# Kernel tuning notes

Hardware: AMD Instinct MI355X
Metric: run time of the kernel (lower is better)

The kernel has to match this reference:

```python
import jax, jax.numpy as jnp
import numpy as np

# static config (matches init_kwargs and spatial_shapes input)
SPATIAL = ((100, 100), (50, 50), (25, 25), (13, 13))  # (H, W) per level
D_MODEL, N_HEADS, N_LEVELS, N_POINTS, D_FFN = 256, 8, 4, 4, 1024
D_HEAD = D_MODEL // N_HEADS
LEN_IN = sum(h * w for h, w in SPATIAL)
LEVEL_START = np.cumsum([0] + [h * w for h, w in SPATIAL])[:-1]


def setup_inputs() -> dict:
    key = jax.random.key(0)
    ks = jax.random.split(key, 12)
    N = 2
    f = lambda k, shape, s=0.02: jax.random.normal(k, shape, jnp.float32) * s
    return {
        "src": jax.random.normal(ks[0], (N, LEN_IN, D_MODEL), jnp.float32),
        "pos": jax.random.normal(ks[1], (N, LEN_IN, D_MODEL), jnp.float32),
        "reference_points": jax.random.uniform(ks[2], (N, LEN_IN, N_LEVELS, 2), jnp.float32),
        "spatial_shapes": jnp.asarray(SPATIAL, jnp.int32),
        "level_start_index": jnp.asarray(LEVEL_START, jnp.int32),
        "W_value": f(ks[3], (D_MODEL, D_MODEL)),
        "b_value": jnp.zeros((D_MODEL,), jnp.float32),
        "W_off": f(ks[4], (D_MODEL, N_HEADS * N_LEVELS * N_POINTS * 2)),
        "b_off": f(ks[5], (N_HEADS * N_LEVELS * N_POINTS * 2,), 0.5),
        "W_attn": f(ks[6], (D_MODEL, N_HEADS * N_LEVELS * N_POINTS)),
        "b_attn": jnp.zeros((N_HEADS * N_LEVELS * N_POINTS,), jnp.float32),
        "W_out": f(ks[7], (D_MODEL, D_MODEL)),
        "b_out": jnp.zeros((D_MODEL,), jnp.float32),
        "W1": f(ks[8], (D_MODEL, D_FFN)),
        "b1": jnp.zeros((D_FFN,), jnp.float32),
        "W2": f(ks[9], (D_FFN, D_MODEL)),
        "b2": jnp.zeros((D_MODEL,), jnp.float32),
        "g1": jnp.ones((D_MODEL,), jnp.float32),
        "be1": jnp.zeros((D_MODEL,), jnp.float32),
        "g2": jnp.ones((D_MODEL,), jnp.float32),
        "be2": jnp.zeros((D_MODEL,), jnp.float32),
    }


def _ln(x, g, b, eps=1e-5):
    mu = x.mean(-1, keepdims=True)
    var = ((x - mu) ** 2).mean(-1, keepdims=True)
    return (x - mu) * jax.lax.rsqrt(var + eps) * g + b


def _bilinear(v, loc, H, W):
    # v: [N, heads, H*W, Dh]; loc: [N, Lq, heads, P, 2] normalized to [0,1]
    # replicates F.grid_sample(align_corners=False, padding_mode='zeros') with grid=2*loc-1
    N, Lq, Hh, P, _ = loc.shape
    x = loc[..., 0] * W - 0.5
    y = loc[..., 1] * H - 0.5
    x0 = jnp.floor(x)
    y0 = jnp.floor(y)
    wx1 = x - x0
    wy1 = y - y0
    x0i = x0.astype(jnp.int32)
    y0i = y0.astype(jnp.int32)
    out = jnp.zeros((N, Lq, Hh, P, v.shape[-1]), v.dtype)
    for dy, dx in ((0, 0), (0, 1), (1, 0), (1, 1)):
        xi = x0i + dx
        yi = y0i + dy
        w = (wx1 if dx else 1.0 - wx1) * (wy1 if dy else 1.0 - wy1)
        valid = (xi >= 0) & (xi < W) & (yi >= 0) & (yi < H)
        idx = jnp.clip(yi, 0, H - 1) * W + jnp.clip(xi, 0, W - 1)  # [N,Lq,Hh,P]
        idx = idx.transpose(0, 2, 1, 3).reshape(N, Hh, Lq * P)
        g = jax.vmap(jax.vmap(lambda vm, im: vm[im]))(v, idx)  # [N,Hh,Lq*P,Dh]
        g = g.reshape(N, Hh, Lq, P, -1).transpose(0, 2, 1, 3, 4)
        out = out + (w * valid)[..., None] * g
    return out


def reference(src, pos, reference_points, spatial_shapes, level_start_index,
              W_value, b_value, W_off, b_off, W_attn, b_attn, W_out, b_out,
              W1, b1, W2, b2, g1, be1, g2, be2):
    N, Lq, _ = src.shape
    value = (src @ W_value + b_value).reshape(N, Lq, N_HEADS, D_HEAD)
    q = src + pos  # with_pos_embed
    off = (q @ W_off + b_off).reshape(N, Lq, N_HEADS, N_LEVELS, N_POINTS, 2)
    attn = (q @ W_attn + b_attn).reshape(N, Lq, N_HEADS, N_LEVELS * N_POINTS)
    attn = jax.nn.softmax(attn, axis=-1).reshape(N, Lq, N_HEADS, N_LEVELS, N_POINTS)
    # offset_normalizer = (W, H) per level
    normalizer = jnp.asarray([[w, h] for h, w in SPATIAL], jnp.float32)
    loc = reference_points[:, :, None, :, None, :] + off / normalizer[None, None, None, :, None, :]
    out = jnp.zeros((N, Lq, N_HEADS, D_HEAD), jnp.float32)
    for l, (H, W) in enumerate(SPATIAL):
        s = int(LEVEL_START[l])
        v_l = value[:, s:s + H * W].transpose(0, 2, 1, 3)  # [N, heads, H*W, Dh]
        samp = _bilinear(v_l, loc[:, :, :, l], H, W)       # [N, Lq, heads, P, Dh]
        out = out + jnp.einsum('nqhp,nqhpc->nqhc', attn[:, :, :, l], samp)
    src2 = out.reshape(N, Lq, D_MODEL) @ W_out + b_out
    x = _ln(src + src2, g1, be1)
    ffn = jax.nn.relu(x @ W1 + b1) @ W2 + b2
    return _ln(x + ffn, g2, be2)
```

## Files before the change

### kernel.cpp

```cpp
#include <hip/hip_runtime.h>
#include <hip/hip_bf16.h>
#include <cstdint>

#define D_MODEL   256
#define N_HEADS   8
#define N_LEVELS  4
#define N_POINTS  4
#define D_FFN     1024
#define D_HEAD    32
#define LEN_IN    13294
#define NBATCH    2
#define M_TOK     (NBATCH * LEN_IN)
#define M_PAD     26624

__constant__ int c_lvl_h[4] = {100, 50, 25, 13};
__constant__ int c_lvl_w[4] = {100, 50, 25, 13};
__constant__ int c_lvl_s[4] = {0, 10000, 12500, 13125};

typedef __attribute__((ext_vector_type(8))) __bf16 bf16x8;
typedef __attribute__((ext_vector_type(4))) __bf16 bf16x4;
typedef __attribute__((ext_vector_type(4))) float  f32x4;
typedef __attribute__((ext_vector_type(4))) uint32_t u32x4;

__device__ __forceinline__ float bflo(uint32_t w) { return __uint_as_float(w << 16); }
__device__ __forceinline__ float bfhi(uint32_t w) { return __uint_as_float(w & 0xffff0000u); }

__device__ __forceinline__ void lds_direct16(const void* g, void* l) {
    __builtin_amdgcn_global_load_lds(
        (const __attribute__((address_space(1))) uint32_t*)(uintptr_t)g,
        (__attribute__((address_space(3))) uint32_t*)(uintptr_t)l,
        16, 0, 0);
}

__global__ __launch_bounds__(256) void prep(
    const float* __restrict__ s0, const float* __restrict__ s1, const float* __restrict__ s2,
    const float* __restrict__ s3, const float* __restrict__ s4, const float* __restrict__ s5,
    __bf16* __restrict__ d0, __bf16* __restrict__ d1, __bf16* __restrict__ d2,
    __bf16* __restrict__ d3, __bf16* __restrict__ d4, __bf16* __restrict__ d5,
    const float* __restrict__ b_off, const float* __restrict__ b_attn,
    float* __restrict__ bias_oa,
    const float4* __restrict__ src, const float4* __restrict__ pos,
    bf16x4* __restrict__ sb, bf16x4* __restrict__ qb, int n4)
{
    const int tid = threadIdx.x;
    const int b = blockIdx.x;
    if (b >= 737) {
        const int i = (b - 737) * 256 + tid;
        if (i >= n4) return;
        const float4 s = src[i];
        const float4 p = pos[i];
        bf16x4 sv = { (__bf16)s.x, (__bf16)s.y, (__bf16)s.z, (__bf16)s.w };
        bf16x4 qv = { (__bf16)(s.x + p.x), (__bf16)(s.y + p.y),
                      (__bf16)(s.z + p.z), (__bf16)(s.w + p.w) };
        sb[i] = sv;
        qb[i] = qv;
        return;
    }
    if (b == 736) {
        if (tid < 256) bias_oa[tid] = b_off[tid];
        if (tid < 128) bias_oa[256 + tid] = b_attn[tid];
        return;
    }
    const int tx = tid & 31;
    const int ty = tid >> 5;
    const int starts[7] = {0, 64, 128, 160, 224, 480, 736};
    const int Ks[6] = {256, 256, 256, 256, 256, 1024};
    const int Ns[6] = {256, 256, 128, 256, 1024, 256};
    const float* srcs[6] = {s0, s1, s2, s3, s4, s5};
    __bf16* dsts[6] = {d0, d1, d2, d3, d4, d5};
    int i = 0;
    while (b >= starts[i + 1]) ++i;
    const int t = b - starts[i];
    const int K = Ks[i], N = Ns[i];
    const float* W = srcs[i];
    __bf16* Wt = dsts[i];
    const int ntx = N >> 5;
    const int n0 = (t % ntx) * 32;
    const int k0 = (t / ntx) * 32;

    __shared__ float tl[32][33];
    #pragma unroll
    for (int j = 0; j < 4; ++j)
        tl[ty + j * 8][tx] = W[(size_t)(k0 + ty + j * 8) * N + n0 + tx];
    __syncthreads();
    #pragma unroll
    for (int j = 0; j < 4; ++j)
        Wt[(size_t)(n0 + ty + j * 8) * K + k0 + tx] = (__bf16)tl[tx][ty + j * 8];
}

template <bool RELU, int K, bool HEADMAJOR>
__device__ __forceinline__ void gemm_core(
    const __bf16* __restrict__ A, const __bf16* __restrict__ Bt,
    const float* __restrict__ bias, __bf16* __restrict__ C,
    int M, int N, int bm, int bn)
{
    __shared__ __bf16 smem[17408];
    __bf16* As = smem;
    __bf16* Bs = smem + 8192;

    const int tid  = threadIdx.x;
    const int lane = tid & 63;
    const int wv   = tid >> 6;
    const int wm   = (wv >> 1) * 64;
    const int wn   = (wv & 1) * 64;
    const int srow = lane >> 2;
    const int skc  = (lane & 3) * 8;
    const int fm   = lane & 15;
    const int fko  = (lane >> 4) * 8;

    f32x4 acc[4][4] = {};

    for (int k0 = 0; k0 < K; k0 += 64) {
        #pragma unroll
        for (int p = 0; p < 2; ++p) {
            #pragma unroll
            for (int c = 0; c < 2; ++c) {
                const int r = wv * 32 + c * 16;
                lds_direct16(A  + (size_t)(bm + r + srow) * K + k0 + p * 32 + skc, As + p * 4096 + r * 32);
                lds_direct16(Bt + (size_t)(bn + r + srow) * K + k0 + p * 32 + skc, Bs + p * 4096 + r * 32);
            }
        }
        __syncthreads();

        #pragma unroll
        for (int p = 0; p < 2; ++p) {
            bf16x8 af[4], bfr[4];
            #pragma unroll
            for (int t = 0; t < 4; ++t) {
                af[t]  = *(const bf16x8*)(As + p * 4096 + (wm + t * 16 + fm) * 32 + fko);
                bfr[t] = *(const bf16x8*)(Bs + p * 4096 + (wn + t * 16 + fm) * 32 + fko);
            }
            #pragma unroll
            for (int mt = 0; mt < 4; ++mt)
                #pragma unroll
                for (int nt = 0; nt < 4; ++nt)
                    acc[mt][nt] = __builtin_amdgcn_mfma_f32_16x16x32_bf16(
                        af[mt], bfr[nt], acc[mt][nt], 0, 0, 0);
        }
        __syncthreads();
    }

    const int ecol = lane & 15;
    const int erow = (lane >> 4) * 4;
    #pragma unroll
    for (int nt = 0; nt < 4; ++nt) {
        const int cl = wn + nt * 16 + ecol;
        const float bv = bias[bn + cl];
        #pragma unroll
        for (int mt = 0; mt < 4; ++mt) {
            #pragma unroll
            for (int r = 0; r < 4; ++r) {
                const int rl = wm + mt * 16 + erow + r;
                float v = acc[mt][nt][r] + bv;
                if (RELU) v = fmaxf(v, 0.f);
                smem[rl * 136 + cl] = (__bf16)v;
            }
        }
    }
    __syncthreads();
    #pragma unroll
    for (int rr = 0; rr < 8; ++rr) {
        const int idx = rr * 256 + tid;
        if (HEADMAJOR) {
            const int plane = idx >> 9;
            const int row   = (idx >> 2) & 127;
            const int ch4   = idx & 3;
            if (bm + row < M)
                *(bf16x8*)(C + ((size_t)((bn >> 5) + plane) * M_PAD + (bm + row)) * 32 + ch4 * 8) =
                    *(const bf16x8*)(smem + row * 136 + plane * 32 + ch4 * 8);
        } else {
            const int row = idx >> 4;
            const int ch  = idx & 15;
            if (bm + row < M)
                *(bf16x8*)(C + (size_t)(bm + row) * N + bn + ch * 8) =
                    *(const bf16x8*)(smem + row * 136 + ch * 8);
        }
    }
}

__global__ __launch_bounds__(256) void gemm_front(
    const __bf16* __restrict__ A0, const __bf16* __restrict__ B0,
    const float* __restrict__ bi0, __bf16* __restrict__ C0,
    const __bf16* __restrict__ A1, const __bf16* __restrict__ B1,
    const float* __restrict__ bi1, __bf16* __restrict__ C1, int M)
{
    const int bx = blockIdx.x;
    if (bx < 2)
        gemm_core<false, 256, true>(A0, B0, bi0, C0, M, 256, blockIdx.y * 128, bx * 128);
    else
        gemm_core<false, 256, false>(A1, B1, bi1, C1, M, 384, blockIdx.y * 128, (bx - 2) * 128);
}

__global__ __launch_bounds__(256) void gemm_ffn1(
    const __bf16* __restrict__ A, const __bf16* __restrict__ Bt,
    const float* __restrict__ bias, __bf16* __restrict__ C, int M)
{
    gemm_core<true, 256, false>(A, Bt, bias, C, M, 1024, blockIdx.y * 128, blockIdx.x * 128);
}

template <typename OutT, int K>
__global__ __launch_bounds__(256, 4) void gemm_ln(
    const __bf16* __restrict__ A, const __bf16* __restrict__ Bt,
    const float* __restrict__ bias, const __bf16* __restrict__ res,
    const float* __restrict__ gamma, const float* __restrict__ beta,
    OutT* __restrict__ Cout, int M)
{
    __shared__ __bf16 smem[2][9216];
    __shared__ float lnsum[32][4];
    __shared__ float lnsq[32][4];
    __shared__ float lnstat[32][2];

    const int tid  = threadIdx.x;
    const int lane = tid & 63;
    const int wv   = tid >> 6;
    const int bm   = blockIdx.x * 32;
    const int wn   = wv * 64;
    const int srow = lane >> 2;
    const int skc  = (lane & 3) * 8;
    const int fm   = lane & 15;
    const int fko  = (lane >> 4) * 8;

    f32x4 acc[2][4] = {};

    auto stage = [&](int b, int k0) {
        __bf16* As = smem[b];
        __bf16* Bs = smem[b] + 1024;
        if (tid < 128)
            lds_direct16(A + (size_t)(bm + (tid >> 2)) * K + k0 + (tid & 3) * 8,
                         As + tid * 8);
        #pragma unroll
        for (int c = 0; c < 4; ++c) {
            const int r = wv * 64 + c * 16;
            lds_direct16(Bt + (size_t)(r + srow) * K + k0 + skc, Bs + r * 32);
        }
    };
    auto compute = [&](int b) {
        const __bf16* As = smem[b];
        const __bf16* Bs = smem[b] + 1024;
        bf16x8 af[2], bfr[4];
        #pragma unroll
        for (int mt = 0; mt < 2; ++mt)
            af[mt] = *(const bf16x8*)(As + (mt * 16 + fm) * 32 + fko);
        #pragma unroll
        for (int nt = 0; nt < 4; ++nt)
            bfr[nt] = *(const bf16x8*)(Bs + (wn + nt * 16 + fm) * 32 + fko);
        #pragma unroll
        for (int mt = 0; mt < 2; ++mt)
            #pragma unroll
            for (int nt = 0; nt < 4; ++nt)
                acc[mt][nt] = __builtin_amdgcn_mfma_f32_16x16x32_bf16(
                    af[mt], bfr[nt], acc[mt][nt], 0, 0, 0);
    };

    stage(0, 0);
    __syncthreads();
    int cur = 0;
    for (int k0 = 32; k0 < K; k0 += 32) {
        stage(cur ^ 1, k0);
        compute(cur);
        __syncthreads();
        cur ^= 1;
    }
    compute(cur);

    const int ecol = lane & 15;
    const int erow = (lane >> 4) * 4;

    float g4[4], b4[4];
    #pragma unroll
    for (int nt = 0; nt < 4; ++nt) {
        const int col = wn + nt * 16 + ecol;
        g4[nt] = gamma[col];
        b4[nt] = beta[col];
        const float bv = bias[col];
        #pragma unroll
        for (int mt = 0; mt < 2; ++mt) {
            #pragma unroll
            for (int r = 0; r < 4; ++r) {
                const int row = bm + mt * 16 + erow + r;
                acc[mt][nt][r] += bv + (float)res[(size_t)row * 256 + col];
            }
        }
    }

    #pragma unroll
    for (int mt = 0; mt < 2; ++mt) {
        #pragma unroll
        for (int r = 0; r < 4; ++r) {
            float s  = acc[mt][0][r] + acc[mt][1][r] + acc[mt][2][r] + acc[mt][3][r];
            float s2 = acc[mt][0][r] * acc[mt][0][r] + acc[mt][1][r] * acc[mt][1][r]
                     + acc[mt][2][r] * acc[mt][2][r] + acc[mt][3][r] * acc[mt][3][r];
            #pragma unroll
            for (int o = 1; o < 16; o <<= 1) {
                s  += __shfl_xor(s, o);
                s2 += __shfl_xor(s2, o);
            }
            if (ecol == 0) {
                const int rl = mt * 16 + erow + r;
                lnsum[rl][wv] = s;
                lnsq[rl][wv]  = s2;
            }
        }
    }
    __syncthreads();
    if (tid < 32) {
        const float s  = lnsum[tid][0] + lnsum[tid][1] + lnsum[tid][2] + lnsum[tid][3];
        const float s2 = lnsq[tid][0] + lnsq[tid][1] + lnsq[tid][2] + lnsq[tid][3];
        const float mu = s * (1.f / 256.f);
        const float var = s2 * (1.f / 256.f) - mu * mu;
        lnstat[tid][0] = mu;
        lnstat[tid][1] = rsqrtf(var + 1e-5f);
    }
    __syncthreads();

    if constexpr (sizeof(OutT) == 2) {
        __bf16* ct = smem[0];
        #pragma unroll
        for (int mt = 0; mt < 2; ++mt) {
            #pragma unroll
            for (int r = 0; r < 4; ++r) {
                const int rl = mt * 16 + erow + r;
                const float mu = lnstat[rl][0];
                const float rs = lnstat[rl][1];
                #pragma unroll
                for (int nt = 0; nt < 4; ++nt) {
                    const int col = wn + nt * 16 + ecol;
                    ct[rl * 264 + col] = (__bf16)((acc[mt][nt][r] - mu) * rs * g4[nt] + b4[nt]);
                }
            }
        }
        __syncthreads();
        #pragma unroll
        for (int rr = 0; rr < 4; ++rr) {
            const int idx = rr * 256 + tid;
            const int row = idx >> 5;
            const int ch  = idx & 31;
            if (bm + row < M)
                *(bf16x8*)((__bf16*)Cout + (size_t)(bm + row) * 256 + ch * 8) =
                    *(const bf16x8*)(ct + row * 264 + ch * 8);
        }
    } else {
        float* ct = (float*)smem[0];
        #pragma unroll
        for (int hf = 0; hf < 2; ++hf) {
            const int mt = hf;
            #pragma unroll
            for (int r = 0; r < 4; ++r) {
                const int rl   = mt * 16 + erow + r;
                const int rloc = erow + r;
                const float mu = lnstat[rl][0];
                const float rs = lnstat[rl][1];
                #pragma unroll
                for (int nt = 0; nt < 4; ++nt) {
                    const int col = wn + nt * 16 + ecol;
                    ct[rloc * 260 + col] = (acc[mt][nt][r] - mu) * rs * g4[nt] + b4[nt];
                }
            }
            __syncthreads();
            #pragma unroll
            for (int rr = 0; rr < 4; ++rr) {
                const int idx = rr * 256 + tid;
                const int row = idx >> 6;
                const int ch  = idx & 63;
                const int grow = bm + hf * 16 + row;
                if (grow < M) {
                    float4 v = *(const float4*)(ct + row * 260 + ch * 4);
                    *(float4*)((float*)Cout + (size_t)grow * 256 + ch * 4) = v;
                }
            }
            __syncthreads();
        }
    }
}

__global__ __launch_bounds__(256) void msda_sample(
    const __bf16* __restrict__ value,
    const __bf16* __restrict__ oa,
    const float* __restrict__ refp,
    __bf16* __restrict__ out)
{
    __shared__ uint32_t sc[32 * 132];
    __shared__ float sw[32][16];

    const int tid = threadIdx.x;
    const int blk = blockIdx.x;

    if (tid < 32) {
        const int t = tid >> 3;
        const int h = tid & 7;
        const int row = blk * 4 + t;
        const __bf16* ap = oa + (size_t)row * 384 + 256 + h * 16;
        const bf16x8 v0 = *(const bf16x8*)ap;
        const bf16x8 v1 = *(const bf16x8*)(ap + 8);
        float e[16];
        #pragma unroll
        for (int i = 0; i < 8; ++i) { e[i] = (float)v0[i]; e[8 + i] = (float)v1[i]; }
        float mx = -1e30f;
        #pragma unroll
        for (int i = 0; i < 16; ++i) mx = fmaxf(mx, e[i]);
        float s = 0.f;
        #pragma unroll
        for (int i = 0; i < 16; ++i) { e[i] = __expf(e[i] - mx); s += e[i]; }
        const float inv = 1.f / s;
        #pragma unroll
        for (int i = 0; i < 16; ++i) sw[tid][i] = e[i] * inv;
    }
    __syncthreads();

    #pragma unroll
    for (int it = 0; it < 2; ++it) {
        const int idx = it * 256 + tid;
        const int t  = idx >> 7;
        const int h  = (idx >> 4) & 7;
        const int lp = idx & 15;
        const int l  = lp >> 2;
        const int row = blk * 4 + t;
        const int Ww = c_lvl_w[l];
        const int Hh = c_lvl_h[l];
        const uint32_t opk = *(const uint32_t*)(oa + (size_t)row * 384 + h * 32 + lp * 2);
        const float ox = bflo(opk), oy = bfhi(opk);
        const float rx = refp[((size_t)row * 4 + l) * 2 + 0];
        const float ry = refp[((size_t)row * 4 + l) * 2 + 1];
        const float x = (rx + ox / (float)Ww) * (float)Ww - 0.5f;
        const float y = (ry + oy / (float)Hh) * (float)Hh - 0.5f;
        const float xf = floorf(x), yf = floorf(y);
        const float fx = x - xf,    fy = y - yf;
        const int x0 = (int)xf, y0 = (int)yf;
        const int n  = (row >= LEN_IN) ? 1 : 0;
        const int lvlbase = n * LEN_IN + c_lvl_s[l];
        const float a = sw[t * 8 + h][lp];
        const int xs = min(max(x0, 0), Ww - 2);
        const int d  = x0 - xs;
        const float wxl = 1.f - fx, wxr = fx;
        const float pw0 = (d == 0) ? wxl : ((d == -1) ? wxr : 0.f);
        const float pw1 = (d == 0) ? wxr : ((d == 1) ? wxl : 0.f);
        uint32_t* p = sc + (t * 8 + h) * 132 + lp * 8;
        #pragma unroll
        for (int dy = 0; dy < 2; ++dy) {
            const int yi = y0 + dy;
            const int yc = min(max(yi, 0), Hh - 1);
            const bool yv = (yi >= 0) & (yi < Hh);
            const float wy = (dy ? fy : 1.f - fy) * (yv ? a : 0.f);
            const uint32_t boff = (uint32_t)(lvlbase + yc * Ww + xs) * 64u;
            u32x4 pk = { boff, __float_as_uint(pw0 * wy), __float_as_uint(pw1 * wy), 0u };
            *(u32x4*)(p + dy * 4) = pk;
        }
    }
    __syncthreads();

    const int t  = tid >> 6;
    const int h  = (tid >> 3) & 7;
    const int c8 = tid & 7;
    const uint32_t* mb = sc + (t * 8 + h) * 132;
    const char* __restrict__ vpb = (const char*)(value + (size_t)h * (M_PAD * 32));
    const uint32_t lsub = (uint32_t)c8 * 16u;
    const bool hi = (c8 >= 4);
    float acc[8] = {};
    #pragma unroll 8
    for (int qd = 0; qd < 32; ++qd) {
        const u32x4 md = *(const u32x4*)(mb + qd * 4);
        const float w = __uint_as_float(hi ? md.z : md.y);
        const u32x4 v = *(const u32x4*)(vpb + (size_t)(md.x + lsub));
        #pragma unroll
        for (int d2 = 0; d2 < 4; ++d2) {
            acc[2 * d2]     += w * bflo(v[d2]);
            acc[2 * d2 + 1] += w * bfhi(v[d2]);
        }
    }
    #pragma unroll
    for (int j = 0; j < 8; ++j) acc[j] += __shfl_xor(acc[j], 4);
    if (c8 < 4) {
        bf16x8 o;
        #pragma unroll
        for (int j = 0; j < 8; ++j) o[j] = (__bf16)acc[j];
        const int orow = blk * 4 + t;
        *(bf16x8*)(out + (size_t)orow * 256 + h * 32 + c8 * 8) = o;
    }
}

extern "C" void kernel_launch(void* const* d_in, const int* in_sizes, int n_in,
                              void* d_out, int out_size, void* d_ws, size_t ws_size,
                              hipStream_t stream)
{
    const float* src     = (const float*)d_in[0];
    const float* pos     = (const float*)d_in[1];
    const float* refp    = (const float*)d_in[2];
    const float* W_value = (const float*)d_in[5];
    const float* b_value = (const float*)d_in[6];
    const float* W_off   = (const float*)d_in[7];
    const float* b_off   = (const float*)d_in[8];
    const float* W_attn  = (const float*)d_in[9];
    const float* b_attn  = (const float*)d_in[10];
    const float* W_out   = (const float*)d_in[11];
    const float* b_out   = (const float*)d_in[12];
    const float* W1      = (const float*)d_in[13];
    const float* b1      = (const float*)d_in[14];
    const float* W2      = (const float*)d_in[15];
    const float* b2      = (const float*)d_in[16];
    const float* g1      = (const float*)d_in[17];
    const float* be1     = (const float*)d_in[18];
    const float* g2      = (const float*)d_in[19];
    const float* be2     = (const float*)d_in[20];
    float* outp = (float*)d_out;

    const int M = M_TOK;
    char* ws = (char*)d_ws;
    const size_t R2 = (size_t)M_PAD * 512;

    __bf16* src_b = (__bf16*)(ws);
    __bf16* q_b   = (__bf16*)(ws + R2);
    __bf16* val_b = (__bf16*)(ws + 2 * R2);
    __bf16* oa    = (__bf16*)(ws + 3 * R2);
    __bf16* samp  = (__bf16*)(ws + 9 * R2 / 2);
    __bf16* x_b   = (__bf16*)(ws + 11 * R2 / 2);
    __bf16* hbuf  = (__bf16*)(ws);
    __bf16* wbase = (__bf16*)(ws + 13 * R2 / 2);
    __bf16* Wt_value = wbase;
    __bf16* Wt_oa    = wbase + 65536;
    __bf16* Wt_out   = wbase + 163840;
    __bf16* Wt1      = wbase + 229376;
    __bf16* Wt2      = wbase + 491520;
    float*  bias_oa  = (float*)(wbase + 753664);

    const dim3 blk(256);
    const int n4 = M * 256 / 4;
    const int gm = M_PAD / 128;

    prep<<<dim3(737 + (n4 + 255) / 256), blk, 0, stream>>>(
        W_value, W_off, W_attn, W_out, W1, W2,
        Wt_value, Wt_oa, Wt_oa + 65536, Wt_out, Wt1, Wt2,
        b_off, b_attn, bias_oa,
        (const float4*)src, (const float4*)pos, (bf16x4*)src_b, (bf16x4*)q_b, n4);

    gemm_front<<<dim3(5, gm), blk, 0, stream>>>(
        src_b, Wt_value, b_value, val_b,
        q_b,   Wt_oa,    bias_oa, oa, M);

    msda_sample<<<dim3(M / 4), blk, 0, stream>>>(val_b, oa, refp, samp);

    gemm_ln<__bf16, 256><<<dim3(M_PAD / 32), blk, 0, stream>>>(
        samp, Wt_out, b_out, src_b, g1, be1, x_b, M);

    gemm_ffn1<<<dim3(8, gm), blk, 0, stream>>>(x_b, Wt1, b1, hbuf, M);

    gemm_ln<float, 1024><<<dim3(M_PAD / 32), blk, 0, stream>>>(
        hbuf, Wt2, b2, x_b, g2, be2, outp, M);
}
```

Before: 299.7 us.

## Make gemm_ln staging wave-private without barriers and regroup msda_sample by head pairs

In gemm_ln, each wave now stages its own copy of the A tile and its own slice of B in shared memory. It uses `s_waitcnt vmcnt` plus scheduling barriers instead of block-wide `__syncthreads`, which removes the barrier stalls in the K loop. The cost is a larger shared-memory footprint, so the launch-bounds occupancy hint drops from 4 to 3 blocks. msda_sample is relaunched on a 2D grid: each block handles 16 tokens for 2 heads rather than 4 tokens for all 8 heads. This is meant to improve locality of value-buffer gathers per head. Out-of-range rows are clamped on read and skipped on write.

```diff
diff --git a/kernel.cpp b/kernel.cpp
--- a/kernel.cpp
+++ b/kernel.cpp
@@ -199,13 +199,13 @@
 }
 
 template <typename OutT, int K>
-__global__ __launch_bounds__(256, 4) void gemm_ln(
+__global__ __launch_bounds__(256, 3) void gemm_ln(
     const __bf16* __restrict__ A, const __bf16* __restrict__ Bt,
     const float* __restrict__ bias, const __bf16* __restrict__ res,
     const float* __restrict__ gamma, const float* __restrict__ beta,
     OutT* __restrict__ Cout, int M)
 {
-    __shared__ __bf16 smem[2][9216];
+    __shared__ __bf16 smem[2][12288];
     __shared__ float lnsum[32][4];
     __shared__ float lnsq[32][4];
     __shared__ float lnstat[32][2];
@@ -223,27 +223,26 @@
     f32x4 acc[2][4] = {};
 
     auto stage = [&](int b, int k0) {
-        __bf16* As = smem[b];
-        __bf16* Bs = smem[b] + 1024;
-        if (tid < 128)
-            lds_direct16(A + (size_t)(bm + (tid >> 2)) * K + k0 + (tid & 3) * 8,
-                         As + tid * 8);
+        __bf16* Asw = smem[b] + wv * 1024;
+        __bf16* Bsw = smem[b] + 4096;
+        lds_direct16(A + (size_t)(bm +  0 + srow) * K + k0 + skc, Asw);
+        lds_direct16(A + (size_t)(bm + 16 + srow) * K + k0 + skc, Asw + 512);
         #pragma unroll
         for (int c = 0; c < 4; ++c) {
             const int r = wv * 64 + c * 16;
-            lds_direct16(Bt + (size_t)(r + srow) * K + k0 + skc, Bs + r * 32);
+            lds_direct16(Bt + (size_t)(r + srow) * K + k0 + skc, Bsw + r * 32);
         }
     };
     auto compute = [&](int b) {
-        const __bf16* As = smem[b];
-        const __bf16* Bs = smem[b] + 1024;
+        const __bf16* Asw = smem[b] + wv * 1024;
+        const __bf16* Bsw = smem[b] + 4096;
         bf16x8 af[2], bfr[4];
         #pragma unroll
         for (int mt = 0; mt < 2; ++mt)
-            af[mt] = *(const bf16x8*)(As + (mt * 16 + fm) * 32 + fko);
+            af[mt] = *(const bf16x8*)(Asw + (mt * 16 + fm) * 32 + fko);
         #pragma unroll
         for (int nt = 0; nt < 4; ++nt)
-            bfr[nt] = *(const bf16x8*)(Bs + (wn + nt * 16 + fm) * 32 + fko);
+            bfr[nt] = *(const bf16x8*)(Bsw + (wn + nt * 16 + fm) * 32 + fko);
         #pragma unroll
         for (int mt = 0; mt < 2; ++mt)
             #pragma unroll
@@ -253,14 +252,16 @@
     };
 
     stage(0, 0);
-    __syncthreads();
     int cur = 0;
     for (int k0 = 32; k0 < K; k0 += 32) {
         stage(cur ^ 1, k0);
+        asm volatile("s_waitcnt vmcnt(6)" ::: "memory");
+        __builtin_amdgcn_sched_barrier(0);
         compute(cur);
-        __syncthreads();
         cur ^= 1;
     }
+    asm volatile("s_waitcnt vmcnt(0)" ::: "memory");
+    __builtin_amdgcn_sched_barrier(0);
     compute(cur);
 
     const int ecol = lane & 15;
@@ -382,13 +383,14 @@
     __shared__ uint32_t sc[32 * 132];
     __shared__ float sw[32][16];
 
-    const int tid = threadIdx.x;
-    const int blk = blockIdx.x;
+    const int tid   = threadIdx.x;
+    const int blk   = blockIdx.x;
+    const int hbase = blockIdx.y * 2;
 
     if (tid < 32) {
-        const int t = tid >> 3;
-        const int h = tid & 7;
-        const int row = blk * 4 + t;
+        const int t = tid >> 1;
+        const int h = hbase + (tid & 1);
+        int row = blk * 16 + t; if (row >= M_TOK) row = M_TOK - 1;
         const __bf16* ap = oa + (size_t)row * 384 + 256 + h * 16;
         const bf16x8 v0 = *(const bf16x8*)ap;
         const bf16x8 v1 = *(const bf16x8*)(ap + 8);
@@ -410,11 +412,12 @@
     #pragma unroll
     for (int it = 0; it < 2; ++it) {
         const int idx = it * 256 + tid;
-        const int t  = idx >> 7;
-        const int h  = (idx >> 4) & 7;
+        const int t  = idx >> 5;
+        const int hl = (idx >> 4) & 1;
         const int lp = idx & 15;
         const int l  = lp >> 2;
-        const int row = blk * 4 + t;
+        const int h  = hbase + hl;
+        int row = blk * 16 + t; if (row >= M_TOK) row = M_TOK - 1;
         const int Ww = c_lvl_w[l];
         const int Hh = c_lvl_h[l];
         const uint32_t opk = *(const uint32_t*)(oa + (size_t)row * 384 + h * 32 + lp * 2);
@@ -428,13 +431,13 @@
         const int x0 = (int)xf, y0 = (int)yf;
         const int n  = (row >= LEN_IN) ? 1 : 0;
         const int lvlbase = n * LEN_IN + c_lvl_s[l];
-        const float a = sw[t * 8 + h][lp];
+        const float a = sw[t * 2 + hl][lp];
         const int xs = min(max(x0, 0), Ww - 2);
         const int d  = x0 - xs;
         const float wxl = 1.f - fx, wxr = fx;
         const float pw0 = (d == 0) ? wxl : ((d == -1) ? wxr : 0.f);
         const float pw1 = (d == 0) ? wxr : ((d == 1) ? wxl : 0.f);
-        uint32_t* p = sc + (t * 8 + h) * 132 + lp * 8;
+        uint32_t* p = sc + (t * 2 + hl) * 132 + lp * 8;
         #pragma unroll
         for (int dy = 0; dy < 2; ++dy) {
             const int yi = y0 + dy;
@@ -448,10 +451,11 @@
     }
     __syncthreads();
 
-    const int t  = tid >> 6;
-    const int h  = (tid >> 3) & 7;
+    const int t  = tid >> 4;
+    const int hl = (tid >> 3) & 1;
     const int c8 = tid & 7;
-    const uint32_t* mb = sc + (t * 8 + h) * 132;
+    const int h  = hbase + hl;
+    const uint32_t* mb = sc + (t * 2 + hl) * 132;
     const char* __restrict__ vpb = (const char*)(value + (size_t)h * (M_PAD * 32));
     const uint32_t lsub = (uint32_t)c8 * 16u;
     const bool hi = (c8 >= 4);
@@ -470,11 +474,13 @@
     #pragma unroll
     for (int j = 0; j < 8; ++j) acc[j] += __shfl_xor(acc[j], 4);
     if (c8 < 4) {
-        bf16x8 o;
-        #pragma unroll
-        for (int j = 0; j < 8; ++j) o[j] = (__bf16)acc[j];
-        const int orow = blk * 4 + t;
-        *(bf16x8*)(out + (size_t)orow * 256 + h * 32 + c8 * 8) = o;
+        const int orow = blk * 16 + t;
+        if (orow < M_TOK) {
+            bf16x8 o;
+            #pragma unroll
+            for (int j = 0; j < 8; ++j) o[j] = (__bf16)acc[j];
+            *(bf16x8*)(out + (size_t)orow * 256 + h * 32 + c8 * 8) = o;
+        }
     }
 }
 
@@ -536,7 +542,7 @@
         src_b, Wt_value, b_value, val_b,
         q_b,   Wt_oa,    bias_oa, oa, M);
 
-    msda_sample<<<dim3(M / 4), blk, 0, stream>>>(val_b, oa, refp, samp);
+    msda_sample<<<dim3((M + 15) / 16, 4), blk, 0, stream>>>(val_b, oa, refp, samp);
 
     gemm_ln<__bf16, 256><<<dim3(M_PAD / 32), blk, 0, stream>>>(
         samp, Wt_out, b_out, src_b, g1, be1, x_b, M);
```

Result: no change. 298.2 us (-0.5%).
